# Performance work log

Hardware: AMD Instinct MI355X
Metric: run time of the kernel (lower is better)

## Reference

```python
import jax, jax.numpy as jnp
import numpy as np
from jax import lax

B = 256; D_IN = 2048; HID = 2048; NSEG = 10; D_CTX = 1024; OUT = 100; NI = 205
KW_PCT = 0.05
K = int(round(KW_PCT * HID))  # 102 winners per sample per layer
W_DENSITY = 0.05      # weight_sparsity = 0.95
DEND_DENSITY = 0.05   # dendrite_weight_sparsity = 0.95


def setup_inputs() -> dict:
    key = jax.random.key(0)
    ks = jax.random.split(key, 16)
    def u(k, shape, bound):
        return jax.random.uniform(k, shape, minval=-bound, maxval=bound, dtype=jnp.float32)
    inp = {}
    inp["x"] = jax.random.normal(ks[0], (B, D_IN), jnp.float32)
    inp["context"] = jax.random.normal(ks[1], (B, D_CTX), jnp.float32)
    # layer 1 FF weights: modified kaiming, input density 1.0 -> bound = 1/sqrt(fan_in)
    inp["W1"] = u(ks[2], (HID, D_IN), 1.0 / np.sqrt(D_IN))
    inp["b1"] = jnp.zeros((HID,), jnp.float32)
    # dendrites: input density 1.0 (context_percent_on=1), weight density 0.05
    dend_bound = 1.0 / np.sqrt(DEND_DENSITY * D_CTX)
    inp["segW1"] = u(ks[3], (HID, NSEG, D_CTX), dend_bound)
    inp["maskW1"] = (jax.random.uniform(ks[4], (HID, D_IN)) < W_DENSITY).astype(jnp.float32)
    inp["maskS1"] = (jax.random.uniform(ks[5], (HID, NSEG, D_CTX)) < DEND_DENSITY).astype(jnp.float32)
    # layer 2 FF weights: input density = kw_percent_on (k-winners upstream)
    inp["W2"] = u(ks[6], (HID, HID), 1.0 / np.sqrt(KW_PCT * HID))
    inp["b2"] = jnp.zeros((HID,), jnp.float32)
    inp["segW2"] = u(ks[7], (HID, NSEG, D_CTX), dend_bound)
    inp["maskW2"] = (jax.random.uniform(ks[8], (HID, HID)) < W_DENSITY).astype(jnp.float32)
    inp["maskS2"] = (jax.random.uniform(ks[9], (HID, NSEG, D_CTX)) < DEND_DENSITY).astype(jnp.float32)
    # Dale (EiDense) output head: non-negative excitatory/inhibitory factors
    s = 1.0 / np.sqrt(HID)
    inp["Wex_out"] = jax.random.uniform(ks[10], (OUT, HID), dtype=jnp.float32) * s
    inp["Wix_out"] = jax.random.uniform(ks[11], (1, HID), dtype=jnp.float32) * s
    inp["Wei_out"] = jax.random.uniform(ks[12], (OUT, 1), dtype=jnp.float32)
    inp["b_out"] = jnp.zeros((OUT,), jnp.float32)
    return inp


def _kwinners(y, k):
    # keep top-k activations per row, zero the rest (boost_strength=0)
    vals, idxs = lax.top_k(y, k)  # [B, k]
    rows = jnp.arange(y.shape[0])[:, None]
    return jnp.zeros_like(y).at[rows, idxs].set(vals)


def _dendritic_layer(x, context, W, b, segW, maskW, maskS):
    # sparse-masked feedforward projection
    y = x @ (W * maskW).T + b  # [B, HID]
    # per-unit dendrite segment activations from context
    d = jnp.einsum('bc,usc->bus', context, segW * maskS)  # [B, HID, NSEG]
    # absolute-max gating: pick segment with max |activation|, gate by sigmoid
    sel = jnp.argmax(jnp.abs(d), axis=-1)  # [B, HID]
    chosen = jnp.take_along_axis(d, sel[..., None], axis=-1)[..., 0]
    y = y * jax.nn.sigmoid(chosen)
    return _kwinners(y, K)


def reference(x, context, W1, b1, segW1, maskW1, maskS1, W2, b2, segW2, maskW2, maskS2, Wex_out, Wix_out, Wei_out, b_out):
    h = _dendritic_layer(x, context, W1, b1, segW1, maskW1, maskS1)
    h = _dendritic_layer(h, context, W2, b2, segW2, maskW2, maskS2)
    # EiDense output head: W = Wex - Wei @ Wix (Dale's law), no output nonlinearity
    W_out = Wex_out - Wei_out @ Wix_out  # [OUT, HID]
    return h @ W_out.T + b_out
```

## Files before the change

### kernel.cpp

```cpp
#include <hip/hip_runtime.h>
#include <math.h>

#define B_SZ   256
#define D_IN   2048
#define HID    2048
#define NSEG   10
#define D_CTX  1024
#define OUT_N  100
#define KWIN   102
#define CAP    256
#define CAPS   128

typedef float f32x4 __attribute__((ext_vector_type(4)));

__device__ __forceinline__ f32x4 ntld4(const float* p) {
  return __builtin_nontemporal_load((const f32x4*)p);
}

__device__ __forceinline__ unsigned f2key(float f) {
  unsigned b = __float_as_uint(f);
  return (b & 0x80000000u) ? ~b : (b | 0x80000000u);
}
__device__ __forceinline__ float key2f(unsigned k) {
  return (k & 0x80000000u) ? __uint_as_float(k & 0x7FFFFFFFu) : __uint_as_float(~k);
}

__global__ __launch_bounds__(256) void transpose2_k(const float* __restrict__ xsrc,
                                                    float* __restrict__ xdst,
                                                    const float* __restrict__ csrc,
                                                    float* __restrict__ cdst) {
  __shared__ float tile[32][33];
  int bid = blockIdx.x;
  const float* src; float* dst; int cols;
  const int NX = (D_IN / 32) * (B_SZ / 32);
  if (bid < NX) { src = xsrc; dst = xdst; cols = D_IN; }
  else { bid -= NX; src = csrc; dst = cdst; cols = D_CTX; }
  int nbx = cols / 32;
  int bx = bid % nbx, by = bid / nbx;
  int c0 = bx * 32, r0 = by * 32;
  int tx = threadIdx.x & 31, ty = threadIdx.x >> 5;
  for (int i = ty; i < 32; i += 8)
    tile[i][tx] = src[(r0 + i) * cols + (c0 + tx)];
  __syncthreads();
  for (int i = ty; i < 32; i += 8)
    dst[(c0 + i) * B_SZ + (r0 + tx)] = tile[tx][i];
}

__device__ __forceinline__ void gather_dot(const float* __restrict__ src,
                                           const float2* pairs, int cnt,
                                           int t4, float out4[4]) {
  float acc[4][4];
#pragma unroll
  for (int s = 0; s < 4; ++s)
#pragma unroll
    for (int i = 0; i < 4; ++i) acc[s][i] = 0.f;
  int j = 0;
  for (; j + 8 <= cnt; j += 8) {
#pragma unroll
    for (int s = 0; s < 8; ++s) {
      float2 p = pairs[j + s];
      const f32x4 cv = *(const f32x4*)(src + (__float_as_int(p.y) << 8) + t4);
      acc[s & 3][0] += cv.x * p.x; acc[s & 3][1] += cv.y * p.x;
      acc[s & 3][2] += cv.z * p.x; acc[s & 3][3] += cv.w * p.x;
    }
  }
  for (; j < cnt; ++j) {
    float2 p = pairs[j];
    const f32x4 cv = *(const f32x4*)(src + (__float_as_int(p.y) << 8) + t4);
    acc[0][0] += cv.x * p.x; acc[0][1] += cv.y * p.x;
    acc[0][2] += cv.z * p.x; acc[0][3] += cv.w * p.x;
  }
#pragma unroll
  for (int i = 0; i < 4; ++i)
    out4[i] = (acc[0][i] + acc[1][i]) + (acc[2][i] + acc[3][i]);
}

__device__ __forceinline__ void load_seg(const float* __restrict__ wrow,
                                         const float* __restrict__ mrow,
                                         f32x4 w[4], f32x4 m[4]) {
  const int t = threadIdx.x & 63;
#pragma unroll
  for (int i = 0; i < 4; ++i) {
    w[i] = ntld4(wrow + 4 * (t + 64 * i));
    m[i] = ntld4(mrow + 4 * (t + 64 * i));
  }
}

__device__ __forceinline__ int store_seg_ballot(const f32x4 w[4], const f32x4 m[4],
                                                float2* pairs) {
  const int t = threadIdx.x & 63;
  const unsigned long long below = (1ull << t) - 1ull;
  int base = 0;
#pragma unroll
  for (int i = 0; i < 4; ++i) {
    const int c = (t + 64 * i) << 2;
    const float wv[4] = {w[i].x, w[i].y, w[i].z, w[i].w};
    const float mv[4] = {m[i].x, m[i].y, m[i].z, m[i].w};
#pragma unroll
    for (int j = 0; j < 4; ++j) {
      bool nz = (mv[j] != 0.f);
      unsigned long long bal = __ballot(nz);
      if (nz) {
        int pos = base + (int)__popcll(bal & below);
        if (pos < CAPS) pairs[pos] = make_float2(wv[j], __int_as_float(c + j));
      }
      base += (int)__popcll(bal);
    }
  }
  __builtin_amdgcn_wave_barrier();
  return base > CAPS ? CAPS : base;
}

__global__ __launch_bounds__(256, 4) void dend_gates_kernel(
    const float* __restrict__ segW1, const float* __restrict__ maskS1,
    const float* __restrict__ segW2, const float* __restrict__ maskS2,
    const float* __restrict__ ctxT,
    float* __restrict__ gate1T, float* __restrict__ gate2T) {
  __shared__ float2 pairs_s[4][CAPS];
  __shared__ float exch[2][64][9];
  const int wave = threadIdx.x >> 6;
  const int t = threadIdx.x & 63, t4 = t * 4;
  const int pidx = wave >> 1;
  const int half = wave & 1;
  const int row = blockIdx.x * 2 + pidx;
  const bool isL1 = (row < HID);
  const int u = isL1 ? row : (row - HID);
  const float* segW = (isL1 ? segW1 : segW2)
                      + (size_t)u * NSEG * D_CTX + (size_t)half * 5 * D_CTX;
  const float* maskS = (isL1 ? maskS1 : maskS2)
                      + (size_t)u * NSEG * D_CTX + (size_t)half * 5 * D_CTX;
  float2* pairs = pairs_s[wave];

  float bestA[4] = {-1.f, -1.f, -1.f, -1.f};
  float chosen[4] = {0.f, 0.f, 0.f, 0.f};

  f32x4 w[4], m[4];
  load_seg(segW, maskS, w, m);
#pragma unroll 1
  for (int s = 0; s < 5; ++s) {
    int cnt = store_seg_ballot(w, m, pairs);
    if (s + 1 < 5)
      load_seg(segW + (s + 1) * D_CTX, maskS + (s + 1) * D_CTX, w, m);
    float d[4];
    gather_dot(ctxT, pairs, cnt, t4, d);
#pragma unroll
    for (int i = 0; i < 4; ++i) {
      float a = fabsf(d[i]);
      if (a > bestA[i]) { bestA[i] = a; chosen[i] = d[i]; }
    }
  }

  if (half) {
#pragma unroll
    for (int i = 0; i < 4; ++i) {
      exch[pidx][t][i] = bestA[i];
      exch[pidx][t][4 + i] = chosen[i];
    }
  }
  __syncthreads();
  if (!half) {
#pragma unroll
    for (int i = 0; i < 4; ++i) {
      float a1 = exch[pidx][t][i];
      if (a1 > bestA[i]) chosen[i] = exch[pidx][t][4 + i];
    }
    float4 g;
    g.x = 1.f / (1.f + expf(-chosen[0]));
    g.y = 1.f / (1.f + expf(-chosen[1]));
    g.z = 1.f / (1.f + expf(-chosen[2]));
    g.w = 1.f / (1.f + expf(-chosen[3]));
    float* gT = isL1 ? gate1T : gate2T;
    *(float4*)(gT + (size_t)u * B_SZ + t4) = g;
  }
}

__global__ __launch_bounds__(256, 4) void ff_kernel(
    const float* __restrict__ W, const float* __restrict__ maskW, const float* __restrict__ b,
    const float* __restrict__ srcT, const float* __restrict__ gateT, float* __restrict__ yT) {
  __shared__ float2 pairs_s[4][CAP];
  const int wave = threadIdx.x >> 6;
  const int t = threadIdx.x & 63, t4 = t * 4;
  const int u = blockIdx.x * 4 + wave;
  float2* pairs = pairs_s[wave];
  const float* wrow = W + (size_t)u * HID;
  const float* mrow = maskW + (size_t)u * HID;
  const unsigned long long below = (1ull << t) - 1ull;
  int base = 0;
  for (int e = t; e < HID / 4; e += 64) {
    f32x4 ww = ntld4(wrow + 4 * e);
    f32x4 mm = ntld4(mrow + 4 * e);
    const float wv[4] = {ww.x, ww.y, ww.z, ww.w};
    const float mv[4] = {mm.x, mm.y, mm.z, mm.w};
    const int c = e << 2;
#pragma unroll
    for (int j = 0; j < 4; ++j) {
      bool nz = (mv[j] != 0.f);
      unsigned long long bal = __ballot(nz);
      if (nz) {
        int pos = base + (int)__popcll(bal & below);
        if (pos < CAP) pairs[pos] = make_float2(wv[j], __int_as_float(c + j));
      }
      base += (int)__popcll(bal);
    }
  }
  __builtin_amdgcn_wave_barrier();
  int cnt = base > CAP ? CAP : base;
  float acc[4];
  gather_dot(srcT, pairs, cnt, t4, acc);
  float bb = b[u];
  float4 g = *(const float4*)(gateT + (size_t)u * B_SZ + t4);
  float4 o;
  o.x = (acc[0] + bb) * g.x; o.y = (acc[1] + bb) * g.y;
  o.z = (acc[2] + bb) * g.z; o.w = (acc[3] + bb) * g.w;
  *(float4*)(yT + (size_t)u * B_SZ + t4) = o;
}

__global__ __launch_bounds__(256) void topk_kernel(const float* __restrict__ yT,
                                                   float* __restrict__ dst, int mode) {
  const int b = blockIdx.x, t = threadIdx.x;
  __shared__ int hist[256];
  __shared__ int sfx[256];
  __shared__ unsigned sPref;
  __shared__ int sRem;
  unsigned myk[8];
#pragma unroll
  for (int i = 0; i < 8; ++i)
    myk[i] = f2key(yT[(size_t)(t * 8 + i) * B_SZ + b]);
  unsigned pref = 0;
  int rem = KWIN;
  for (int shift = 24; shift >= 0; shift -= 8) {
    hist[t] = 0;
    __syncthreads();
    unsigned hiMask = (shift == 24) ? 0u : (0xFFFFFFFFu << (shift + 8));
#pragma unroll
    for (int i = 0; i < 8; ++i) {
      unsigned k = myk[i];
      if ((k & hiMask) == pref) atomicAdd(&hist[(k >> shift) & 255], 1);
    }
    __syncthreads();
    sfx[t] = hist[t];
    __syncthreads();
    for (int off = 1; off < 256; off <<= 1) {
      int add = (t + off < 256) ? sfx[t + off] : 0;
      __syncthreads();
      sfx[t] += add;
      __syncthreads();
    }
    int s_incl = sfx[t];
    int s_excl = (t == 255) ? 0 : sfx[t + 1];
    if (s_incl >= rem && s_excl < rem) {
      sPref = pref | (((unsigned)t) << shift);
      sRem = rem - s_excl;
    }
    __syncthreads();
    pref = sPref;
    rem = sRem;
    __syncthreads();
  }
  int eq = 0;
#pragma unroll
  for (int i = 0; i < 8; ++i) eq += (myk[i] == pref) ? 1 : 0;
  sfx[t] = eq;
  __syncthreads();
  for (int off = 1; off < 256; off <<= 1) {
    int add = (t >= off) ? sfx[t - off] : 0;
    __syncthreads();
    sfx[t] += add;
    __syncthreads();
  }
  int excl = sfx[t] - eq;
  int taken = 0;
#pragma unroll
  for (int i = 0; i < 8; ++i) {
    unsigned k = myk[i];
    bool keep;
    if (k > pref) keep = true;
    else if (k == pref) { keep = (excl + taken) < rem; taken++; }
    else keep = false;
    float f = keep ? key2f(k) : 0.f;
    int uu = t * 8 + i;
    if (mode == 0) dst[(size_t)uu * B_SZ + b] = f;
    else dst[(size_t)b * HID + uu] = f;
  }
}

__global__ __launch_bounds__(256) void out_kernel(
    const float* __restrict__ h2, const float* __restrict__ Wex, const float* __restrict__ Wix,
    const float* __restrict__ Wei, const float* __restrict__ bo, float* __restrict__ out) {
  const int b = blockIdx.x, t = threadIdx.x;
  __shared__ float hrow[HID];
  __shared__ float red[256];
  float part = 0.f;
#pragma unroll
  for (int i = 0; i < 8; ++i) {
    int u = t + 256 * i;
    float v = h2[(size_t)b * HID + u];
    hrow[u] = v;
    part += v * Wix[u];
  }
  red[t] = part;
  __syncthreads();
  for (int off = 128; off > 0; off >>= 1) {
    if (t < off) red[t] += red[t + off];
    __syncthreads();
  }
  float S = red[0];
  const int w = t >> 6, l = t & 63;
  for (int o = w; o < OUT_N; o += 4) {
    float acc = 0.f;
    const float* wr = Wex + (size_t)o * HID;
#pragma unroll
    for (int q = 0; q < HID / 64; ++q) acc += hrow[l + 64 * q] * wr[l + 64 * q];
    for (int off = 32; off > 0; off >>= 1) acc += __shfl_down(acc, off, 64);
    if (l == 0) out[(size_t)b * OUT_N + o] = acc - Wei[o] * S + bo[o];
  }
}

extern "C" void kernel_launch(void* const* d_in, const int* in_sizes, int n_in,
                              void* d_out, int out_size, void* d_ws, size_t ws_size,
                              hipStream_t stream) {
  const float* x      = (const float*)d_in[0];
  const float* ctx    = (const float*)d_in[1];
  const float* W1     = (const float*)d_in[2];
  const float* b1     = (const float*)d_in[3];
  const float* segW1  = (const float*)d_in[4];
  const float* maskW1 = (const float*)d_in[5];
  const float* maskS1 = (const float*)d_in[6];
  const float* W2     = (const float*)d_in[7];
  const float* b2     = (const float*)d_in[8];
  const float* segW2  = (const float*)d_in[9];
  const float* maskW2 = (const float*)d_in[10];
  const float* maskS2 = (const float*)d_in[11];
  const float* Wex    = (const float*)d_in[12];
  const float* Wix    = (const float*)d_in[13];
  const float* Wei    = (const float*)d_in[14];
  const float* bo     = (const float*)d_in[15];
  float* out = (float*)d_out;
  float* ws = (float*)d_ws;

  float* xT     = ws;
  float* ctxT   = ws + 524288;
  float* y1T    = ws + 786432;
  float* gate2T = ws + 1310720;
  float* slotA  = ws + 1835008;
  float* h2     = ws + 2359296;
  float* gate1T = slotA;
  float* y2T    = slotA;

  transpose2_k<<<768, 256, 0, stream>>>(x, xT, ctx, ctxT);
  dend_gates_kernel<<<2 * HID / 2, 256, 0, stream>>>(segW1, maskS1, segW2, maskS2,
                                                     ctxT, gate1T, gate2T);
  ff_kernel<<<HID / 4, 256, 0, stream>>>(W1, maskW1, b1, xT, gate1T, y1T);
  topk_kernel<<<B_SZ, 256, 0, stream>>>(y1T, y1T, 0);
  ff_kernel<<<HID / 4, 256, 0, stream>>>(W2, maskW2, b2, y1T, gate2T, y2T);
  topk_kernel<<<B_SZ, 256, 0, stream>>>(y2T, h2, 1);
  out_kernel<<<B_SZ, 256, 0, stream>>>(h2, Wex, Wix, Wei, bo, out);
}
```

Baseline: 524.4 us.

## Gather dendrite weights only at masked indices; single-wave bitwise top-k

The dendrite gating kernel no longer streams the full segment weight rows. It compacts only the mask indices and then gathers the matching weights during the dot product, cutting weight reads to roughly the nonzero fraction at the cost of scattered loads. Occupancy hint drops from 4 to 3. The top-k kernel is rewritten as a single 64-thread wave doing a 32-step bitwise threshold search with ballots, replacing shared-memory radix histograms and block barriers. This uses more registers and serial work per sample.

```diff
diff --git a/kernel.cpp b/kernel.cpp
--- a/kernel.cpp
+++ b/kernel.cpp
@@ -75,26 +75,20 @@
     out4[i] = (acc[0][i] + acc[1][i]) + (acc[2][i] + acc[3][i]);
 }
 
-__device__ __forceinline__ void load_seg(const float* __restrict__ wrow,
-                                         const float* __restrict__ mrow,
-                                         f32x4 w[4], f32x4 m[4]) {
+__device__ __forceinline__ void load_mask(const float* __restrict__ mrow, f32x4 m[4]) {
   const int t = threadIdx.x & 63;
 #pragma unroll
-  for (int i = 0; i < 4; ++i) {
-    w[i] = ntld4(wrow + 4 * (t + 64 * i));
-    m[i] = ntld4(mrow + 4 * (t + 64 * i));
-  }
-}
-
-__device__ __forceinline__ int store_seg_ballot(const f32x4 w[4], const f32x4 m[4],
-                                                float2* pairs) {
+  for (int i = 0; i < 4; ++i) m[i] = ntld4(mrow + 4 * (t + 64 * i));
+}
+
+__device__ __forceinline__ int compact_idx_ballot(const f32x4 m[4], int* idx) {
   const int t = threadIdx.x & 63;
   const unsigned long long below = (1ull << t) - 1ull;
+  __builtin_amdgcn_wave_barrier();
   int base = 0;
 #pragma unroll
   for (int i = 0; i < 4; ++i) {
     const int c = (t + 64 * i) << 2;
-    const float wv[4] = {w[i].x, w[i].y, w[i].z, w[i].w};
     const float mv[4] = {m[i].x, m[i].y, m[i].z, m[i].w};
 #pragma unroll
     for (int j = 0; j < 4; ++j) {
@@ -102,7 +96,7 @@
       unsigned long long bal = __ballot(nz);
       if (nz) {
         int pos = base + (int)__popcll(bal & below);
-        if (pos < CAPS) pairs[pos] = make_float2(wv[j], __int_as_float(c + j));
+        if (pos < CAPS) idx[pos] = c + j;
       }
       base += (int)__popcll(bal);
     }
@@ -111,12 +105,44 @@
   return base > CAPS ? CAPS : base;
 }
 
-__global__ __launch_bounds__(256, 4) void dend_gates_kernel(
+__device__ __forceinline__ void gather_dot_w(const float* __restrict__ src,
+                                             const float* __restrict__ wrow,
+                                             const int* idx, int cnt,
+                                             int t4, float out4[4]) {
+  float acc[4][4];
+#pragma unroll
+  for (int s = 0; s < 4; ++s)
+#pragma unroll
+    for (int i = 0; i < 4; ++i) acc[s][i] = 0.f;
+  int j = 0;
+  for (; j + 8 <= cnt; j += 8) {
+#pragma unroll
+    for (int s = 0; s < 8; ++s) {
+      int c = idx[j + s];
+      float wv = wrow[c];
+      const f32x4 cv = *(const f32x4*)(src + (c << 8) + t4);
+      acc[s & 3][0] += cv.x * wv; acc[s & 3][1] += cv.y * wv;
+      acc[s & 3][2] += cv.z * wv; acc[s & 3][3] += cv.w * wv;
+    }
+  }
+  for (; j < cnt; ++j) {
+    int c = idx[j];
+    float wv = wrow[c];
+    const f32x4 cv = *(const f32x4*)(src + (c << 8) + t4);
+    acc[0][0] += cv.x * wv; acc[0][1] += cv.y * wv;
+    acc[0][2] += cv.z * wv; acc[0][3] += cv.w * wv;
+  }
+#pragma unroll
+  for (int i = 0; i < 4; ++i)
+    out4[i] = (acc[0][i] + acc[1][i]) + (acc[2][i] + acc[3][i]);
+}
+
+__global__ __launch_bounds__(256, 3) void dend_gates_kernel(
     const float* __restrict__ segW1, const float* __restrict__ maskS1,
     const float* __restrict__ segW2, const float* __restrict__ maskS2,
     const float* __restrict__ ctxT,
     float* __restrict__ gate1T, float* __restrict__ gate2T) {
-  __shared__ float2 pairs_s[4][CAPS];
+  __shared__ int idx_s[4][CAPS];
   __shared__ float exch[2][64][9];
   const int wave = threadIdx.x >> 6;
   const int t = threadIdx.x & 63, t4 = t * 4;
@@ -129,20 +155,20 @@
                       + (size_t)u * NSEG * D_CTX + (size_t)half * 5 * D_CTX;
   const float* maskS = (isL1 ? maskS1 : maskS2)
                       + (size_t)u * NSEG * D_CTX + (size_t)half * 5 * D_CTX;
-  float2* pairs = pairs_s[wave];
+  int* idx = idx_s[wave];
 
   float bestA[4] = {-1.f, -1.f, -1.f, -1.f};
   float chosen[4] = {0.f, 0.f, 0.f, 0.f};
 
-  f32x4 w[4], m[4];
-  load_seg(segW, maskS, w, m);
+  f32x4 m[4];
+  load_mask(maskS, m);
 #pragma unroll 1
   for (int s = 0; s < 5; ++s) {
-    int cnt = store_seg_ballot(w, m, pairs);
+    int cnt = compact_idx_ballot(m, idx);
     if (s + 1 < 5)
-      load_seg(segW + (s + 1) * D_CTX, maskS + (s + 1) * D_CTX, w, m);
+      load_mask(maskS + (s + 1) * D_CTX, m);
     float d[4];
-    gather_dot(ctxT, pairs, cnt, t4, d);
+    gather_dot_w(ctxT, segW + s * D_CTX, idx, cnt, t4, d);
 #pragma unroll
     for (int i = 0; i < 4; ++i) {
       float a = fabsf(d[i]);
@@ -215,70 +241,44 @@
   *(float4*)(yT + (size_t)u * B_SZ + t4) = o;
 }
 
-__global__ __launch_bounds__(256) void topk_kernel(const float* __restrict__ yT,
-                                                   float* __restrict__ dst, int mode) {
+__global__ __launch_bounds__(64) void topk_kernel(const float* __restrict__ yT,
+                                                  float* __restrict__ dst, int mode) {
   const int b = blockIdx.x, t = threadIdx.x;
-  __shared__ int hist[256];
-  __shared__ int sfx[256];
-  __shared__ unsigned sPref;
-  __shared__ int sRem;
-  unsigned myk[8];
-#pragma unroll
-  for (int i = 0; i < 8; ++i)
-    myk[i] = f2key(yT[(size_t)(t * 8 + i) * B_SZ + b]);
-  unsigned pref = 0;
-  int rem = KWIN;
-  for (int shift = 24; shift >= 0; shift -= 8) {
-    hist[t] = 0;
-    __syncthreads();
-    unsigned hiMask = (shift == 24) ? 0u : (0xFFFFFFFFu << (shift + 8));
-#pragma unroll
-    for (int i = 0; i < 8; ++i) {
-      unsigned k = myk[i];
-      if ((k & hiMask) == pref) atomicAdd(&hist[(k >> shift) & 255], 1);
-    }
-    __syncthreads();
-    sfx[t] = hist[t];
-    __syncthreads();
-    for (int off = 1; off < 256; off <<= 1) {
-      int add = (t + off < 256) ? sfx[t + off] : 0;
-      __syncthreads();
-      sfx[t] += add;
-      __syncthreads();
-    }
-    int s_incl = sfx[t];
-    int s_excl = (t == 255) ? 0 : sfx[t + 1];
-    if (s_incl >= rem && s_excl < rem) {
-      sPref = pref | (((unsigned)t) << shift);
-      sRem = rem - s_excl;
-    }
-    __syncthreads();
-    pref = sPref;
-    rem = sRem;
-    __syncthreads();
-  }
-  int eq = 0;
-#pragma unroll
-  for (int i = 0; i < 8; ++i) eq += (myk[i] == pref) ? 1 : 0;
-  sfx[t] = eq;
-  __syncthreads();
-  for (int off = 1; off < 256; off <<= 1) {
-    int add = (t >= off) ? sfx[t - off] : 0;
-    __syncthreads();
-    sfx[t] += add;
-    __syncthreads();
-  }
-  int excl = sfx[t] - eq;
-  int taken = 0;
-#pragma unroll
-  for (int i = 0; i < 8; ++i) {
-    unsigned k = myk[i];
-    bool keep;
-    if (k > pref) keep = true;
-    else if (k == pref) { keep = (excl + taken) < rem; taken++; }
-    else keep = false;
-    float f = keep ? key2f(k) : 0.f;
-    int uu = t * 8 + i;
+  unsigned k[32];
+#pragma unroll
+  for (int i = 0; i < 32; ++i)
+    k[i] = f2key(yT[(size_t)(t * 32 + i) * B_SZ + b]);
+  unsigned T = 0u;
+  for (int bit = 31; bit >= 0; --bit) {
+    unsigned cand = T | (1u << bit);
+    int cnt = 0;
+#pragma unroll
+    for (int i = 0; i < 32; ++i)
+      cnt += (int)__popcll(__ballot(k[i] >= cand));
+    if (cnt >= KWIN) T = cand;
+  }
+  int cntGT = 0;
+#pragma unroll
+  for (int i = 0; i < 32; ++i)
+    cntGT += (int)__popcll(__ballot(k[i] > T));
+  const int rem = KWIN - cntGT;
+  int e = 0;
+#pragma unroll
+  for (int i = 0; i < 32; ++i) e += (k[i] == T) ? 1 : 0;
+  int scan = e;
+#pragma unroll
+  for (int off = 1; off < 64; off <<= 1) {
+    int v = __shfl_up(scan, off, 64);
+    if (t >= off) scan += v;
+  }
+  int tk = scan - e;
+#pragma unroll
+  for (int i = 0; i < 32; ++i) {
+    bool eq = (k[i] == T);
+    bool keep = (k[i] > T) || (eq && tk < rem);
+    tk += eq ? 1 : 0;
+    float f = keep ? key2f(k[i]) : 0.f;
+    int uu = t * 32 + i;
     if (mode == 0) dst[(size_t)uu * B_SZ + b] = f;
     else dst[(size_t)b * HID + uu] = f;
   }
@@ -351,8 +351,8 @@
   dend_gates_kernel<<<2 * HID / 2, 256, 0, stream>>>(segW1, maskS1, segW2, maskS2,
                                                      ctxT, gate1T, gate2T);
   ff_kernel<<<HID / 4, 256, 0, stream>>>(W1, maskW1, b1, xT, gate1T, y1T);
-  topk_kernel<<<B_SZ, 256, 0, stream>>>(y1T, y1T, 0);
+  topk_kernel<<<B_SZ, 64, 0, stream>>>(y1T, y1T, 0);
   ff_kernel<<<HID / 4, 256, 0, stream>>>(W2, maskW2, b2, y1T, gate2T, y2T);
-  topk_kernel<<<B_SZ, 256, 0, stream>>>(y2T, h2, 1);
+  topk_kernel<<<B_SZ, 64, 0, stream>>>(y2T, h2, 1);
   out_kernel<<<B_SZ, 256, 0, stream>>>(h2, Wex, Wix, Wei, bo, out);
 }
```

New measurement: 546.8 us. +4.3%, slower.

## Fuse layer-1 FF into dendrite kernel, split FF rows across waves, fuse top-k with output

Applied to the files above, without the earlier changes.

Layer-1's feedforward sparse dot is folded into the dendrite gating kernel, so the gated y1 is written directly and the gate1 round trip and one launch disappear. Layer 2's FF kernel now splits each row across two waves, each handling half the columns, with a shared-memory reduction, which doubles the block count. The final top-k is fused into the output head, so h2 is never written to global memory. The dendrite loads also lose their software prefetch, since segment loads now happen inside the compaction step, which may expose memory latency. Each half-row compaction is capped at 128 entries, which risks silently dropping nonzeros on denser rows.

```diff
diff --git a/kernel.cpp b/kernel.cpp
--- a/kernel.cpp
+++ b/kernel.cpp
@@ -8,7 +8,6 @@
 #define D_CTX  1024
 #define OUT_N  100
 #define KWIN   102
-#define CAP    256
 #define CAPS   128
 
 typedef float f32x4 __attribute__((ext_vector_type(4)));
@@ -46,56 +45,21 @@
     dst[(c0 + i) * B_SZ + (r0 + tx)] = tile[tx][i];
 }
 
-__device__ __forceinline__ void gather_dot(const float* __restrict__ src,
-                                           const float2* pairs, int cnt,
-                                           int t4, float out4[4]) {
-  float acc[4][4];
-#pragma unroll
-  for (int s = 0; s < 4; ++s)
-#pragma unroll
-    for (int i = 0; i < 4; ++i) acc[s][i] = 0.f;
-  int j = 0;
-  for (; j + 8 <= cnt; j += 8) {
-#pragma unroll
-    for (int s = 0; s < 8; ++s) {
-      float2 p = pairs[j + s];
-      const f32x4 cv = *(const f32x4*)(src + (__float_as_int(p.y) << 8) + t4);
-      acc[s & 3][0] += cv.x * p.x; acc[s & 3][1] += cv.y * p.x;
-      acc[s & 3][2] += cv.z * p.x; acc[s & 3][3] += cv.w * p.x;
-    }
-  }
-  for (; j < cnt; ++j) {
-    float2 p = pairs[j];
-    const f32x4 cv = *(const f32x4*)(src + (__float_as_int(p.y) << 8) + t4);
-    acc[0][0] += cv.x * p.x; acc[0][1] += cv.y * p.x;
-    acc[0][2] += cv.z * p.x; acc[0][3] += cv.w * p.x;
-  }
-#pragma unroll
-  for (int i = 0; i < 4; ++i)
-    out4[i] = (acc[0][i] + acc[1][i]) + (acc[2][i] + acc[3][i]);
-}
-
-__device__ __forceinline__ void load_seg(const float* __restrict__ wrow,
-                                         const float* __restrict__ mrow,
-                                         f32x4 w[4], f32x4 m[4]) {
-  const int t = threadIdx.x & 63;
-#pragma unroll
-  for (int i = 0; i < 4; ++i) {
-    w[i] = ntld4(wrow + 4 * (t + 64 * i));
-    m[i] = ntld4(mrow + 4 * (t + 64 * i));
-  }
-}
-
-__device__ __forceinline__ int store_seg_ballot(const f32x4 w[4], const f32x4 m[4],
-                                                float2* pairs) {
+__device__ __forceinline__ int compact_pairs_1024(const float* __restrict__ wrow,
+                                                  const float* __restrict__ mrow,
+                                                  int coff, float2* pairs) {
   const int t = threadIdx.x & 63;
   const unsigned long long below = (1ull << t) - 1ull;
+  __builtin_amdgcn_wave_barrier();
   int base = 0;
 #pragma unroll
   for (int i = 0; i < 4; ++i) {
-    const int c = (t + 64 * i) << 2;
-    const float wv[4] = {w[i].x, w[i].y, w[i].z, w[i].w};
-    const float mv[4] = {m[i].x, m[i].y, m[i].z, m[i].w};
+    const int e = t + 64 * i;
+    f32x4 ww = ntld4(wrow + 4 * e);
+    f32x4 mm = ntld4(mrow + 4 * e);
+    const float wv[4] = {ww.x, ww.y, ww.z, ww.w};
+    const float mv[4] = {mm.x, mm.y, mm.z, mm.w};
+    const int c = (e << 2) + coff;
 #pragma unroll
     for (int j = 0; j < 4; ++j) {
       bool nz = (mv[j] != 0.f);
@@ -111,13 +75,43 @@
   return base > CAPS ? CAPS : base;
 }
 
-__global__ __launch_bounds__(256, 4) void dend_gates_kernel(
+__device__ __forceinline__ void gather_dot(const float* __restrict__ src,
+                                           const float2* pairs, int cnt,
+                                           int t4, float out4[4]) {
+  float acc[4][4];
+#pragma unroll
+  for (int s = 0; s < 4; ++s)
+#pragma unroll
+    for (int i = 0; i < 4; ++i) acc[s][i] = 0.f;
+  int j = 0;
+  for (; j + 8 <= cnt; j += 8) {
+#pragma unroll
+    for (int s = 0; s < 8; ++s) {
+      float2 p = pairs[j + s];
+      const f32x4 cv = *(const f32x4*)(src + (__float_as_int(p.y) << 8) + t4);
+      acc[s & 3][0] += cv.x * p.x; acc[s & 3][1] += cv.y * p.x;
+      acc[s & 3][2] += cv.z * p.x; acc[s & 3][3] += cv.w * p.x;
+    }
+  }
+  for (; j < cnt; ++j) {
+    float2 p = pairs[j];
+    const f32x4 cv = *(const f32x4*)(src + (__float_as_int(p.y) << 8) + t4);
+    acc[0][0] += cv.x * p.x; acc[0][1] += cv.y * p.x;
+    acc[0][2] += cv.z * p.x; acc[0][3] += cv.w * p.x;
+  }
+#pragma unroll
+  for (int i = 0; i < 4; ++i)
+    out4[i] = (acc[0][i] + acc[1][i]) + (acc[2][i] + acc[3][i]);
+}
+
+__global__ __launch_bounds__(256, 4) void dendff_kernel(
+    const float* __restrict__ W1, const float* __restrict__ maskW1, const float* __restrict__ b1,
     const float* __restrict__ segW1, const float* __restrict__ maskS1,
     const float* __restrict__ segW2, const float* __restrict__ maskS2,
-    const float* __restrict__ ctxT,
-    float* __restrict__ gate1T, float* __restrict__ gate2T) {
+    const float* __restrict__ xT, const float* __restrict__ ctxT,
+    float* __restrict__ y1T, float* __restrict__ gate2T) {
   __shared__ float2 pairs_s[4][CAPS];
-  __shared__ float exch[2][64][9];
+  __shared__ float exch[2][64][13];
   const int wave = threadIdx.x >> 6;
   const int t = threadIdx.x & 63, t4 = t * 4;
   const int pidx = wave >> 1;
@@ -134,13 +128,9 @@
   float bestA[4] = {-1.f, -1.f, -1.f, -1.f};
   float chosen[4] = {0.f, 0.f, 0.f, 0.f};
 
-  f32x4 w[4], m[4];
-  load_seg(segW, maskS, w, m);
 #pragma unroll 1
   for (int s = 0; s < 5; ++s) {
-    int cnt = store_seg_ballot(w, m, pairs);
-    if (s + 1 < 5)
-      load_seg(segW + (s + 1) * D_CTX, maskS + (s + 1) * D_CTX, w, m);
+    int cnt = compact_pairs_1024(segW + s * D_CTX, maskS + s * D_CTX, 0, pairs);
     float d[4];
     gather_dot(ctxT, pairs, cnt, t4, d);
 #pragma unroll
@@ -150,11 +140,20 @@
     }
   }
 
+  float ffp[4] = {0.f, 0.f, 0.f, 0.f};
+  if (isL1) {
+    const int off = half * 1024;
+    int cnt = compact_pairs_1024(W1 + (size_t)u * D_IN + off,
+                                 maskW1 + (size_t)u * D_IN + off, off, pairs);
+    gather_dot(xT, pairs, cnt, t4, ffp);
+  }
+
   if (half) {
 #pragma unroll
     for (int i = 0; i < 4; ++i) {
       exch[pidx][t][i] = bestA[i];
       exch[pidx][t][4 + i] = chosen[i];
+      exch[pidx][t][8 + i] = ffp[i];
     }
   }
   __syncthreads();
@@ -163,56 +162,56 @@
     for (int i = 0; i < 4; ++i) {
       float a1 = exch[pidx][t][i];
       if (a1 > bestA[i]) chosen[i] = exch[pidx][t][4 + i];
-    }
-    float4 g;
-    g.x = 1.f / (1.f + expf(-chosen[0]));
-    g.y = 1.f / (1.f + expf(-chosen[1]));
-    g.z = 1.f / (1.f + expf(-chosen[2]));
-    g.w = 1.f / (1.f + expf(-chosen[3]));
-    float* gT = isL1 ? gate1T : gate2T;
-    *(float4*)(gT + (size_t)u * B_SZ + t4) = g;
-  }
-}
-
-__global__ __launch_bounds__(256, 4) void ff_kernel(
-    const float* __restrict__ W, const float* __restrict__ maskW, const float* __restrict__ b,
-    const float* __restrict__ srcT, const float* __restrict__ gateT, float* __restrict__ yT) {
-  __shared__ float2 pairs_s[4][CAP];
+      ffp[i] += exch[pidx][t][8 + i];
+    }
+    if (isL1) {
+      float bb = b1[u];
+      float4 o;
+      o.x = (ffp[0] + bb) / (1.f + expf(-chosen[0]));
+      o.y = (ffp[1] + bb) / (1.f + expf(-chosen[1]));
+      o.z = (ffp[2] + bb) / (1.f + expf(-chosen[2]));
+      o.w = (ffp[3] + bb) / (1.f + expf(-chosen[3]));
+      *(float4*)(y1T + (size_t)u * B_SZ + t4) = o;
+    } else {
+      float4 g;
+      g.x = 1.f / (1.f + expf(-chosen[0]));
+      g.y = 1.f / (1.f + expf(-chosen[1]));
+      g.z = 1.f / (1.f + expf(-chosen[2]));
+      g.w = 1.f / (1.f + expf(-chosen[3]));
+      *(float4*)(gate2T + (size_t)u * B_SZ + t4) = g;
+    }
+  }
+}
+
+__global__ __launch_bounds__(256, 4) void ff2_kernel(
+    const float* __restrict__ W2, const float* __restrict__ maskW2, const float* __restrict__ b2,
+    const float* __restrict__ h1T, const float* __restrict__ gate2T, float* __restrict__ y2T) {
+  __shared__ float2 pairs_s[4][CAPS];
+  __shared__ float exch[2][64][5];
   const int wave = threadIdx.x >> 6;
   const int t = threadIdx.x & 63, t4 = t * 4;
-  const int u = blockIdx.x * 4 + wave;
-  float2* pairs = pairs_s[wave];
-  const float* wrow = W + (size_t)u * HID;
-  const float* mrow = maskW + (size_t)u * HID;
-  const unsigned long long below = (1ull << t) - 1ull;
-  int base = 0;
-  for (int e = t; e < HID / 4; e += 64) {
-    f32x4 ww = ntld4(wrow + 4 * e);
-    f32x4 mm = ntld4(mrow + 4 * e);
-    const float wv[4] = {ww.x, ww.y, ww.z, ww.w};
-    const float mv[4] = {mm.x, mm.y, mm.z, mm.w};
-    const int c = e << 2;
-#pragma unroll
-    for (int j = 0; j < 4; ++j) {
-      bool nz = (mv[j] != 0.f);
-      unsigned long long bal = __ballot(nz);
-      if (nz) {
-        int pos = base + (int)__popcll(bal & below);
-        if (pos < CAP) pairs[pos] = make_float2(wv[j], __int_as_float(c + j));
-      }
-      base += (int)__popcll(bal);
-    }
-  }
-  __builtin_amdgcn_wave_barrier();
-  int cnt = base > CAP ? CAP : base;
+  const int pidx = wave >> 1, half = wave & 1;
+  const int u = blockIdx.x * 2 + pidx;
+  const int off = half * 1024;
+  int cnt = compact_pairs_1024(W2 + (size_t)u * HID + off,
+                               maskW2 + (size_t)u * HID + off, off, pairs_s[wave]);
   float acc[4];
-  gather_dot(srcT, pairs, cnt, t4, acc);
-  float bb = b[u];
-  float4 g = *(const float4*)(gateT + (size_t)u * B_SZ + t4);
-  float4 o;
-  o.x = (acc[0] + bb) * g.x; o.y = (acc[1] + bb) * g.y;
-  o.z = (acc[2] + bb) * g.z; o.w = (acc[3] + bb) * g.w;
-  *(float4*)(yT + (size_t)u * B_SZ + t4) = o;
+  gather_dot(h1T, pairs_s[wave], cnt, t4, acc);
+  if (half) {
+#pragma unroll
+    for (int i = 0; i < 4; ++i) exch[pidx][t][i] = acc[i];
+  }
+  __syncthreads();
+  if (!half) {
+#pragma unroll
+    for (int i = 0; i < 4; ++i) acc[i] += exch[pidx][t][i];
+    float bb = b2[u];
+    float4 g = *(const float4*)(gate2T + (size_t)u * B_SZ + t4);
+    float4 o;
+    o.x = (acc[0] + bb) * g.x; o.y = (acc[1] + bb) * g.y;
+    o.z = (acc[2] + bb) * g.z; o.w = (acc[3] + bb) * g.w;
+    *(float4*)(y2T + (size_t)u * B_SZ + t4) = o;
+  }
 }
 
 __global__ __launch_bounds__(256) void topk_kernel(const float* __restrict__ yT,
@@ -284,19 +283,76 @@
   }
 }
 
-__global__ __launch_bounds__(256) void out_kernel(
-    const float* __restrict__ h2, const float* __restrict__ Wex, const float* __restrict__ Wix,
+__global__ __launch_bounds__(256) void topkout_kernel(
+    const float* __restrict__ yT, const float* __restrict__ Wex, const float* __restrict__ Wix,
     const float* __restrict__ Wei, const float* __restrict__ bo, float* __restrict__ out) {
   const int b = blockIdx.x, t = threadIdx.x;
+  __shared__ int hist[256];
+  __shared__ int sfx[256];
+  __shared__ unsigned sPref;
+  __shared__ int sRem;
   __shared__ float hrow[HID];
   __shared__ float red[256];
+  unsigned myk[8];
+#pragma unroll
+  for (int i = 0; i < 8; ++i)
+    myk[i] = f2key(yT[(size_t)(t * 8 + i) * B_SZ + b]);
+  unsigned pref = 0;
+  int rem = KWIN;
+  for (int shift = 24; shift >= 0; shift -= 8) {
+    hist[t] = 0;
+    __syncthreads();
+    unsigned hiMask = (shift == 24) ? 0u : (0xFFFFFFFFu << (shift + 8));
+#pragma unroll
+    for (int i = 0; i < 8; ++i) {
+      unsigned k = myk[i];
+      if ((k & hiMask) == pref) atomicAdd(&hist[(k >> shift) & 255], 1);
+    }
+    __syncthreads();
+    sfx[t] = hist[t];
+    __syncthreads();
+    for (int off = 1; off < 256; off <<= 1) {
+      int add = (t + off < 256) ? sfx[t + off] : 0;
+      __syncthreads();
+      sfx[t] += add;
+      __syncthreads();
+    }
+    int s_incl = sfx[t];
+    int s_excl = (t == 255) ? 0 : sfx[t + 1];
+    if (s_incl >= rem && s_excl < rem) {
+      sPref = pref | (((unsigned)t) << shift);
+      sRem = rem - s_excl;
+    }
+    __syncthreads();
+    pref = sPref;
+    rem = sRem;
+    __syncthreads();
+  }
+  int eq = 0;
+#pragma unroll
+  for (int i = 0; i < 8; ++i) eq += (myk[i] == pref) ? 1 : 0;
+  sfx[t] = eq;
+  __syncthreads();
+  for (int off = 1; off < 256; off <<= 1) {
+    int add = (t >= off) ? sfx[t - off] : 0;
+    __syncthreads();
+    sfx[t] += add;
+    __syncthreads();
+  }
+  int excl = sfx[t] - eq;
+  int taken = 0;
   float part = 0.f;
 #pragma unroll
   for (int i = 0; i < 8; ++i) {
-    int u = t + 256 * i;
-    float v = h2[(size_t)b * HID + u];
-    hrow[u] = v;
-    part += v * Wix[u];
+    unsigned k = myk[i];
+    bool keep;
+    if (k > pref) keep = true;
+    else if (k == pref) { keep = (excl + taken) < rem; taken++; }
+    else keep = false;
+    float f = keep ? key2f(k) : 0.f;
+    int uu = t * 8 + i;
+    hrow[uu] = f;
+    part += f * Wix[uu];
   }
   red[t] = part;
   __syncthreads();
@@ -342,17 +398,12 @@
   float* ctxT   = ws + 524288;
   float* y1T    = ws + 786432;
   float* gate2T = ws + 1310720;
-  float* slotA  = ws + 1835008;
-  float* h2     = ws + 2359296;
-  float* gate1T = slotA;
-  float* y2T    = slotA;
+  float* y2T    = ws + 1835008;
 
   transpose2_k<<<768, 256, 0, stream>>>(x, xT, ctx, ctxT);
-  dend_gates_kernel<<<2 * HID / 2, 256, 0, stream>>>(segW1, maskS1, segW2, maskS2,
-                                                     ctxT, gate1T, gate2T);
-  ff_kernel<<<HID / 4, 256, 0, stream>>>(W1, maskW1, b1, xT, gate1T, y1T);
+  dendff_kernel<<<2 * HID / 2, 256, 0, stream>>>(W1, maskW1, b1, segW1, maskS1,
+                                                 segW2, maskS2, xT, ctxT, y1T, gate2T);
   topk_kernel<<<B_SZ, 256, 0, stream>>>(y1T, y1T, 0);
-  ff_kernel<<<HID / 4, 256, 0, stream>>>(W2, maskW2, b2, y1T, gate2T, y2T);
-  topk_kernel<<<B_SZ, 256, 0, stream>>>(y2T, h2, 1);
-  out_kernel<<<B_SZ, 256, 0, stream>>>(h2, Wex, Wix, Wei, bo, out);
-}
+  ff2_kernel<<<HID / 2, 256, 0, stream>>>(W2, maskW2, b2, y1T, gate2T, y2T);
+  topkout_kernel<<<B_SZ, 256, 0, stream>>>(y2T, Wex, Wix, Wei, bo, out);
+}
```

Result: faster. 488.8 us (-6.8%).
